# Kernel tuning notes

Hardware: AMD Instinct MI355X
Metric: run time of the kernel (lower is better)

Reference implementation:

```python
import jax, jax.numpy as jnp
import numpy as np

_SAMPLING_EPS = 1e-5
EOS_PROB_RATIO = 100.0
MIN_PROB_THRESHOLD = 0.001
MIX_RATIO = 0.5
EOS_TOKEN_ID = 2


def setup_inputs() -> dict:
    key = jax.random.key(0)
    k1, k2, k3, k4 = jax.random.split(key, 4)
    B, V = 256, 128000
    logits = jax.random.normal(k1, (B, V), dtype=jnp.float32) * 3.0
    # keep temperature away from 0 so the random-sampling path is exercised
    temperature = 0.2 + 1.3 * jax.random.uniform(k2, (B,), dtype=jnp.float32)
    top_p = 0.5 + 0.5 * jax.random.uniform(k3, (B,), dtype=jnp.float32)
    token_lengths = jax.random.randint(k4, (V,), 0, 20).astype(jnp.int32)
    return {
        "logits": logits,
        "temperature": temperature,
        "top_p": top_p,
        "token_lengths": token_lengths,
        "top_k": 50,
    }


def _apply_top_k_top_p(logits, top_k, top_p):
    """vLLM-style: ascending sort, top-k threshold, top-p cumulative mask, scatter back."""
    idx = jnp.argsort(logits, axis=-1)  # ascending
    lsort = jnp.take_along_axis(logits, idx, axis=-1)
    V = logits.shape[-1]
    # top-k: keep only the last top_k (largest) entries
    kth = lsort[:, V - top_k][:, None]
    lsort = jnp.where(lsort < kth, -jnp.inf, lsort)
    # top-p: mask low-cumulative-probability prefix (ascending order)
    probs = jax.nn.softmax(lsort, axis=-1)
    csum = jnp.cumsum(probs, axis=-1)
    pmask = csum <= (1.0 - top_p[:, None])
    pmask = pmask.at[:, -1].set(False)  # always keep the top token
    lsort = jnp.where(pmask, -jnp.inf, lsort)
    # scatter back to original token order
    inv = jnp.argsort(idx, axis=-1)
    return jnp.take_along_axis(lsort, inv, axis=-1)


def _longest_word_sample(logits, token_lengths, k, mix_ratio, eos_token_id):
    topk_logits, topk_idx = jax.lax.top_k(logits, k)  # [B,k]
    prob = jax.nn.softmax(topk_logits, axis=-1)
    lens = token_lengths[jnp.clip(topk_idx, 0, token_lengths.shape[0] - 1)].astype(jnp.float32)
    length_score = jax.nn.softmax(lens, axis=-1)
    mix = (1.0 - mix_ratio) * prob + mix_ratio * length_score
    mix = jnp.where(prob >= MIN_PROB_THRESHOLD, mix, -jnp.inf)
    # EOS threshold rule
    eos_in_topk = (topk_idx == eos_token_id) & jnp.isfinite(topk_logits)
    rows_with_eos = eos_in_topk.any(axis=-1, keepdims=True)
    eos_prob = jnp.sum(prob * eos_in_topk, axis=-1, keepdims=True)
    eos_thresh = jnp.maximum(eos_prob / EOS_PROB_RATIO, 0.005)
    valid = prob >= eos_thresh
    mix = jnp.where(valid | ~rows_with_eos, mix, -jnp.inf)
    best = jnp.argmax(mix, axis=-1)  # [B]
    chosen = jnp.take_along_axis(topk_idx, best[:, None], axis=-1)[:, 0]
    return chosen


def reference(logits, temperature, top_p, token_lengths, top_k):
    greedy = jnp.argmax(logits, axis=-1)
    scaled = logits / temperature[:, None]
    filtered = _apply_top_k_top_p(scaled, top_k, top_p)
    rnd = _longest_word_sample(filtered, token_lengths, top_k, MIX_RATIO, EOS_TOKEN_ID)
    sampled = jnp.where(temperature < _SAMPLING_EPS, greedy, rnd)
    return sampled.astype(jnp.int32)
```

## Files before the change

kernel.cpp:

```cpp
#include <hip/hip_runtime.h>
#include <stdint.h>
#include <math.h>

#define THREADS 1024
#define NBINS 8192
#define BIN_SHIFT 19
#define CAND_MAX 2048
#define MAXK 64
#define BATCH 16

__device__ __forceinline__ uint32_t fkey(float f) {
    uint32_t b = __float_as_uint(f);
    return (b & 0x80000000u) ? ~b : (b | 0x80000000u);
}
__device__ __forceinline__ float fval(uint32_t k) {
    uint32_t b = (k & 0x80000000u) ? (k & 0x7FFFFFFFu) : ~k;
    return __uint_as_float(b);
}

__global__ __launch_bounds__(THREADS, 1) void sampler_kernel(
    const float* __restrict__ logits,
    const float* __restrict__ temperature,
    const float* __restrict__ top_p,
    const int* __restrict__ token_lengths,
    const int* __restrict__ top_k_ptr,
    int* __restrict__ out, int V)
{
    const int row = blockIdx.x;
    const int tid = threadIdx.x;
    int K = *top_k_ptr;
    if (K < 1) K = 1;
    if (K > MAXK) K = MAXK;

    __shared__ uint32_t s_hist[NBINS];
    __shared__ uint32_t s_chunk[THREADS];
    __shared__ unsigned long long s_cand[CAND_MAX];
    __shared__ float s_vals[MAXK];
    __shared__ int s_idx[MAXK];
    __shared__ int s_slot[MAXK];
    __shared__ int s_T, s_cnt;

    for (int i = tid; i < NBINS; i += THREADS) s_hist[i] = 0u;
    if (tid == 0) s_cnt = 0;
    __syncthreads();

    const float* rowbase = logits + (size_t)row * (size_t)V;
    const int nv = V >> 2;
    const float4* rowp = reinterpret_cast<const float4*>(rowbase);
    const int jmax = nv - 1;

    for (int base = tid; base < nv; base += THREADS * BATCH) {
        float4 x[BATCH];
        #pragma unroll
        for (int b = 0; b < BATCH; ++b) {
            int j = base + b * THREADS;
            x[b] = rowp[(j < jmax) ? j : jmax];
        }
        #pragma unroll
        for (int b = 0; b < BATCH; ++b) {
            const int j = base + b * THREADS;
            if (j < nv) {
                atomicAdd(&s_hist[fkey(x[b].x) >> BIN_SHIFT], 1u);
                atomicAdd(&s_hist[fkey(x[b].y) >> BIN_SHIFT], 1u);
                atomicAdd(&s_hist[fkey(x[b].z) >> BIN_SHIFT], 1u);
                atomicAdd(&s_hist[fkey(x[b].w) >> BIN_SHIFT], 1u);
            }
        }
    }
    __syncthreads();

    const int CHUNK = NBINS / THREADS;
    {
        uint32_t cs = 0;
        const int base = tid * CHUNK;
        #pragma unroll
        for (int b = 0; b < CHUNK; ++b) cs += s_hist[base + b];
        s_chunk[tid] = cs;
    }
    __syncthreads();
    for (int off = 1; off < THREADS; off <<= 1) {
        uint32_t v = (tid + off < THREADS) ? s_chunk[tid + off] : 0u;
        __syncthreads();
        s_chunk[tid] += v;
        __syncthreads();
    }
    {
        uint32_t suf  = s_chunk[tid];
        uint32_t sufn = (tid + 1 < THREADS) ? s_chunk[tid + 1] : 0u;
        if (suf >= (uint32_t)K && sufn < (uint32_t)K) {
            uint32_t acc = sufn;
            int T = tid * CHUNK;
            for (int b = tid * CHUNK + CHUNK - 1; b >= tid * CHUNK; --b) {
                acc += s_hist[b];
                if (acc >= (uint32_t)K) { T = b; break; }
            }
            s_T = T;
        }
    }
    __syncthreads();

    const uint32_t T = (uint32_t)s_T;
    for (int base = tid; base < nv; base += THREADS * BATCH) {
        float4 x[BATCH];
        #pragma unroll
        for (int b = 0; b < BATCH; ++b) {
            int j = base + b * THREADS;
            x[b] = rowp[(j < jmax) ? j : jmax];
        }
        #pragma unroll
        for (int b = 0; b < BATCH; ++b) {
            const int j = base + b * THREADS;
            if (j < nv) {
                const uint32_t j4 = (uint32_t)(j << 2);
                uint32_t k;
                k = fkey(x[b].x); if ((k >> BIN_SHIFT) >= T) { int p = atomicAdd(&s_cnt, 1); if (p < CAND_MAX) s_cand[p] = ((unsigned long long)k << 32) | (uint32_t)~(j4 + 0u); }
                k = fkey(x[b].y); if ((k >> BIN_SHIFT) >= T) { int p = atomicAdd(&s_cnt, 1); if (p < CAND_MAX) s_cand[p] = ((unsigned long long)k << 32) | (uint32_t)~(j4 + 1u); }
                k = fkey(x[b].z); if ((k >> BIN_SHIFT) >= T) { int p = atomicAdd(&s_cnt, 1); if (p < CAND_MAX) s_cand[p] = ((unsigned long long)k << 32) | (uint32_t)~(j4 + 2u); }
                k = fkey(x[b].w); if ((k >> BIN_SHIFT) >= T) { int p = atomicAdd(&s_cnt, 1); if (p < CAND_MAX) s_cand[p] = ((unsigned long long)k << 32) | (uint32_t)~(j4 + 3u); }
            }
        }
    }
    __syncthreads();

    const int M = min(s_cnt, CAND_MAX);
    for (int t = tid; t < M; t += THREADS) {
        const unsigned long long mine = s_cand[t];
        int rank = 0;
        for (int j = 0; j < M; ++j) rank += (s_cand[j] > mine) ? 1 : 0;
        if (rank < MAXK) {
            s_idx[rank]  = (int)(~(uint32_t)mine);
            s_vals[rank] = fval((uint32_t)(mine >> 32));
        }
    }
    __syncthreads();

    if (tid >= 64) return;

    const float temp = temperature[row];
    const float tp   = top_p[row];

    const float a0 = s_vals[0] / temp;
    float e = 0.f;
    int myidx = -1;
    if (tid < K) {
        myidx = s_idx[tid];
        e = expf(s_vals[tid] / temp - a0);
    }
    float sum = e;
    #pragma unroll
    for (int off = 1; off < 64; off <<= 1) sum += __shfl_xor(sum, off, 64);
    const float p1 = e / sum;

    float cs = p1;
    #pragma unroll
    for (int off = 1; off < 64; off <<= 1) {
        float o = __shfl_down(cs, off, 64);
        cs += (tid + off < 64) ? o : 0.f;
    }
    const float lim = 1.0f - tp;
    const bool keep = (tid < K) && (tid == 0 || cs > lim);
    const int S = __popcll(__ballot(keep));

    float e2 = (tid < S) ? e : 0.f;
    float sum2 = e2;
    #pragma unroll
    for (int off = 1; off < 64; off <<= 1) sum2 += __shfl_xor(sum2, off, 64);
    const float p2 = e2 / sum2;

    const bool is_eos = (tid < S) && (myidx == 2);
    float eosp = is_eos ? p2 : 0.f;
    #pragma unroll
    for (int off = 1; off < 64; off <<= 1) eosp += __shfl_xor(eosp, off, 64);
    const bool has_eos = (__ballot(is_eos) != 0ull);
    const float eth = fmaxf(eosp / 100.0f, 0.005f);

    if (tid < S) s_slot[tid] = myidx;
    __builtin_amdgcn_wave_barrier();
    if (tid == 0) {
        unsigned long long m0 = 0ull, m1 = 0ull;
        for (int i = 0; i < S; ++i) {
            int id = s_idx[i];
            if (id < 64) m0 |= 1ull << id;
            else if (id < 128) m1 |= 1ull << (id - 64);
        }
        int nxt = 0;
        for (int i = S; i < K; ++i) {
            while ((nxt < 64) ? ((m0 >> nxt) & 1ull) : ((m1 >> (nxt - 64)) & 1ull)) nxt++;
            s_slot[i] = nxt++;
        }
    }
    __builtin_amdgcn_wave_barrier();

    float len = -INFINITY;
    if (tid < K) {
        int id = s_slot[tid];
        id = (id < 0) ? 0 : ((id >= V) ? V - 1 : id);
        len = (float)token_lengths[id];
    }
    float lmax = len;
    #pragma unroll
    for (int off = 1; off < 64; off <<= 1) lmax = fmaxf(lmax, __shfl_xor(lmax, off, 64));
    float el = (tid < K) ? expf(len - lmax) : 0.f;
    float lsum = el;
    #pragma unroll
    for (int off = 1; off < 64; off <<= 1) lsum += __shfl_xor(lsum, off, 64);
    const float ls = el / lsum;

    float mix = -INFINITY;
    if (tid < S) {
        mix = 0.5f * p2 + 0.5f * ls;
        if (!(p2 >= 0.001f)) mix = -INFINITY;
        if (has_eos && !(p2 >= eth)) mix = -INFINITY;
    }
    float bm = mix; int bi = tid;
    #pragma unroll
    for (int off = 1; off < 64; off <<= 1) {
        float om = __shfl_xor(bm, off, 64);
        int   oi = __shfl_xor(bi, off, 64);
        if (om > bm || (om == bm && oi < bi)) { bm = om; bi = oi; }
    }

    if (tid == 0) {
        int chosen = s_slot[bi];
        if (temp < 1e-5f) chosen = s_idx[0];
        out[row] = chosen;
    }
}

extern "C" void kernel_launch(void* const* d_in, const int* in_sizes, int n_in,
                              void* d_out, int out_size, void* d_ws, size_t ws_size,
                              hipStream_t stream) {
    const float* logits        = (const float*)d_in[0];
    const float* temperature   = (const float*)d_in[1];
    const float* top_p         = (const float*)d_in[2];
    const int*   token_lengths = (const int*)d_in[3];
    const int*   top_k_ptr     = (const int*)d_in[4];
    int* outp = (int*)d_out;

    const int B = in_sizes[1];
    const int V = in_sizes[3];

    sampler_kernel<<<B, THREADS, 0, stream>>>(logits, temperature, top_p,
                                              token_lengths, top_k_ptr, outp, V);
}
```

Before: 56.24 us.

## Stream logits through per-wave LDS ring via async global_load_lds and shuffle-based scan

Both passes over the row now use async global-to-LDS loads (global_load_lds) into a per-wave 4-slot ring buffer, with vmcnt waits, instead of batched float4 register loads. The goal is to overlap global memory latency with LDS atomics while cutting register pressure. The 1024-thread suffix scan, which needed many block-wide barriers, is replaced by wave-level shuffles plus one small cross-wave scan. CAND_MAX is reduced to make room for the staging buffer. The risk is that only three loads are in flight per wave, which may be less memory-level parallelism than the old 16-deep batches.

After: 51.55 us. -8.3%, faster.

```diff
diff --git a/kernel.cpp b/kernel.cpp
--- a/kernel.cpp
+++ b/kernel.cpp
@@ -3,11 +3,12 @@
 #include <math.h>
 
 #define THREADS 1024
+#define NWAVES 16
 #define NBINS 8192
 #define BIN_SHIFT 19
-#define CAND_MAX 2048
+#define CAND_MAX 1536
 #define MAXK 64
-#define BATCH 16
+#define RING 4
 
 __device__ __forceinline__ uint32_t fkey(float f) {
     uint32_t b = __float_as_uint(f);
@@ -16,6 +17,13 @@
 __device__ __forceinline__ float fval(uint32_t k) {
     uint32_t b = (k & 0x80000000u) ? (k & 0x7FFFFFFFu) : ~k;
     return __uint_as_float(b);
+}
+
+__device__ __forceinline__ void gload_lds16(const float* g, uint32_t* lds) {
+    __builtin_amdgcn_global_load_lds(
+        (const __attribute__((address_space(1))) void*)(const void*)g,
+        (__attribute__((address_space(3))) void*)(void*)lds,
+        16, 0, 0);
 }
 
 __global__ __launch_bounds__(THREADS, 1) void sampler_kernel(
@@ -26,18 +34,20 @@
     const int* __restrict__ top_k_ptr,
     int* __restrict__ out, int V)
 {
-    const int row = blockIdx.x;
-    const int tid = threadIdx.x;
+    const int row  = blockIdx.x;
+    const int tid  = threadIdx.x;
+    const int lane = tid & 63;
+    const int wid  = tid >> 6;
     int K = *top_k_ptr;
     if (K < 1) K = 1;
     if (K > MAXK) K = MAXK;
 
+    __shared__ __align__(16) uint32_t s_stage[NWAVES * RING * 256];
     __shared__ uint32_t s_hist[NBINS];
-    __shared__ uint32_t s_chunk[THREADS];
     __shared__ unsigned long long s_cand[CAND_MAX];
+    __shared__ uint32_t s_wsum[NWAVES], s_wtail[NWAVES];
     __shared__ float s_vals[MAXK];
-    __shared__ int s_idx[MAXK];
-    __shared__ int s_slot[MAXK];
+    __shared__ int s_idx[MAXK], s_slot[MAXK];
     __shared__ int s_T, s_cnt;
 
     for (int i = tid; i < NBINS; i += THREADS) s_hist[i] = 0u;
@@ -45,52 +55,74 @@
     __syncthreads();
 
     const float* rowbase = logits + (size_t)row * (size_t)V;
-    const int nv = V >> 2;
-    const float4* rowp = reinterpret_cast<const float4*>(rowbase);
-    const int jmax = nv - 1;
-
-    for (int base = tid; base < nv; base += THREADS * BATCH) {
-        float4 x[BATCH];
+    const int NREAL = (V + 255) >> 8;
+    const int NITER = (NREAL + NWAVES - 1) / NWAVES;
+    const int lastg = V - 4;
+    uint32_t* mystage = &s_stage[wid * (RING * 256)];
+
+    #pragma unroll
+    for (int k = 0; k < RING - 1; ++k) {
+        int ci = wid + NWAVES * k;
+        int c  = (ci < NREAL - 1) ? ci : (NREAL - 1);
+        int g  = c * 256 + lane * 4;
+        g = (g < lastg) ? g : lastg;
+        gload_lds16(rowbase + g, mystage + k * 256);
+    }
+    for (int i = 0; i < NITER; ++i) {
+        asm volatile("s_waitcnt vmcnt(2)" ::: "memory");
+        const uint32_t* sp = mystage + (i & (RING - 1)) * 256 + lane * 4;
+        float4 x = *reinterpret_cast<const float4*>(sp);
+        const int g0 = (wid + NWAVES * i) * 256 + lane * 4;
+        if (g0 < V) {
+            atomicAdd(&s_hist[fkey(x.x) >> BIN_SHIFT], 1u);
+            atomicAdd(&s_hist[fkey(x.y) >> BIN_SHIFT], 1u);
+            atomicAdd(&s_hist[fkey(x.z) >> BIN_SHIFT], 1u);
+            atomicAdd(&s_hist[fkey(x.w) >> BIN_SHIFT], 1u);
+        }
+        {
+            int ci = wid + NWAVES * (i + RING - 1);
+            int c  = (ci < NREAL - 1) ? ci : (NREAL - 1);
+            int g  = c * 256 + lane * 4;
+            g = (g < lastg) ? g : lastg;
+            gload_lds16(rowbase + g, mystage + ((i + RING - 1) & (RING - 1)) * 256);
+        }
+    }
+    asm volatile("s_waitcnt vmcnt(0)" ::: "memory");
+    __syncthreads();
+
+    const int CH = NBINS / THREADS;
+    uint32_t cs = 0;
+    {
+        const int b0 = tid * CH;
         #pragma unroll
-        for (int b = 0; b < BATCH; ++b) {
-            int j = base + b * THREADS;
-            x[b] = rowp[(j < jmax) ? j : jmax];
-        }
+        for (int b = 0; b < CH; ++b) cs += s_hist[b0 + b];
+    }
+    uint32_t suf = cs;
+    #pragma unroll
+    for (int off = 1; off < 64; off <<= 1) {
+        uint32_t o = __shfl_down(suf, off, 64);
+        suf += (lane + off < 64) ? o : 0u;
+    }
+    if (lane == 0) s_wsum[wid] = suf;
+    __syncthreads();
+    if (wid == 0 && lane < NWAVES) {
+        uint32_t t = s_wsum[lane];
+        uint32_t s = t;
         #pragma unroll
-        for (int b = 0; b < BATCH; ++b) {
-            const int j = base + b * THREADS;
-            if (j < nv) {
-                atomicAdd(&s_hist[fkey(x[b].x) >> BIN_SHIFT], 1u);
-                atomicAdd(&s_hist[fkey(x[b].y) >> BIN_SHIFT], 1u);
-                atomicAdd(&s_hist[fkey(x[b].z) >> BIN_SHIFT], 1u);
-                atomicAdd(&s_hist[fkey(x[b].w) >> BIN_SHIFT], 1u);
-            }
-        }
-    }
-    __syncthreads();
-
-    const int CHUNK = NBINS / THREADS;
+        for (int off = 1; off < NWAVES; off <<= 1) {
+            uint32_t o = __shfl_down(s, off, 64);
+            s += (lane + off < NWAVES) ? o : 0u;
+        }
+        s_wtail[lane] = s - t;
+    }
+    __syncthreads();
     {
-        uint32_t cs = 0;
-        const int base = tid * CHUNK;
-        #pragma unroll
-        for (int b = 0; b < CHUNK; ++b) cs += s_hist[base + b];
-        s_chunk[tid] = cs;
-    }
-    __syncthreads();
-    for (int off = 1; off < THREADS; off <<= 1) {
-        uint32_t v = (tid + off < THREADS) ? s_chunk[tid + off] : 0u;
-        __syncthreads();
-        s_chunk[tid] += v;
-        __syncthreads();
-    }
-    {
-        uint32_t suf  = s_chunk[tid];
-        uint32_t sufn = (tid + 1 < THREADS) ? s_chunk[tid + 1] : 0u;
-        if (suf >= (uint32_t)K && sufn < (uint32_t)K) {
+        uint32_t sufg = suf + s_wtail[wid];
+        uint32_t sufn = sufg - cs;
+        if (sufg >= (uint32_t)K && sufn < (uint32_t)K) {
             uint32_t acc = sufn;
-            int T = tid * CHUNK;
-            for (int b = tid * CHUNK + CHUNK - 1; b >= tid * CHUNK; --b) {
+            int T = tid * CH;
+            for (int b = tid * CH + CH - 1; b >= tid * CH; --b) {
                 acc += s_hist[b];
                 if (acc >= (uint32_t)K) { T = b; break; }
             }
@@ -100,29 +132,38 @@
     __syncthreads();
 
     const uint32_t T = (uint32_t)s_T;
-    for (int base = tid; base < nv; base += THREADS * BATCH) {
-        float4 x[BATCH];
-        #pragma unroll
-        for (int b = 0; b < BATCH; ++b) {
-            int j = base + b * THREADS;
-            x[b] = rowp[(j < jmax) ? j : jmax];
-        }
-        #pragma unroll
-        for (int b = 0; b < BATCH; ++b) {
-            const int j = base + b * THREADS;
-            if (j < nv) {
-                const uint32_t j4 = (uint32_t)(j << 2);
-                uint32_t k;
-                k = fkey(x[b].x); if ((k >> BIN_SHIFT) >= T) { int p = atomicAdd(&s_cnt, 1); if (p < CAND_MAX) s_cand[p] = ((unsigned long long)k << 32) | (uint32_t)~(j4 + 0u); }
-                k = fkey(x[b].y); if ((k >> BIN_SHIFT) >= T) { int p = atomicAdd(&s_cnt, 1); if (p < CAND_MAX) s_cand[p] = ((unsigned long long)k << 32) | (uint32_t)~(j4 + 1u); }
-                k = fkey(x[b].z); if ((k >> BIN_SHIFT) >= T) { int p = atomicAdd(&s_cnt, 1); if (p < CAND_MAX) s_cand[p] = ((unsigned long long)k << 32) | (uint32_t)~(j4 + 2u); }
-                k = fkey(x[b].w); if ((k >> BIN_SHIFT) >= T) { int p = atomicAdd(&s_cnt, 1); if (p < CAND_MAX) s_cand[p] = ((unsigned long long)k << 32) | (uint32_t)~(j4 + 3u); }
-            }
-        }
-    }
-    __syncthreads();
-
-    const int M = min(s_cnt, CAND_MAX);
+    #pragma unroll
+    for (int k = 0; k < RING - 1; ++k) {
+        int ci = wid + NWAVES * k;
+        int c  = (ci < NREAL - 1) ? ci : (NREAL - 1);
+        int g  = c * 256 + lane * 4;
+        g = (g < lastg) ? g : lastg;
+        gload_lds16(rowbase + g, mystage + k * 256);
+    }
+    for (int i = 0; i < NITER; ++i) {
+        asm volatile("s_waitcnt vmcnt(2)" ::: "memory");
+        const uint32_t* sp = mystage + (i & (RING - 1)) * 256 + lane * 4;
+        float4 x = *reinterpret_cast<const float4*>(sp);
+        const int g0 = (wid + NWAVES * i) * 256 + lane * 4;
+        if (g0 < V) {
+            uint32_t k0;
+            k0 = fkey(x.x); if ((k0 >> BIN_SHIFT) >= T) { int p = atomicAdd(&s_cnt, 1); if (p < CAND_MAX) s_cand[p] = ((unsigned long long)k0 << 32) | (uint32_t)~(uint32_t)(g0 + 0); }
+            k0 = fkey(x.y); if ((k0 >> BIN_SHIFT) >= T) { int p = atomicAdd(&s_cnt, 1); if (p < CAND_MAX) s_cand[p] = ((unsigned long long)k0 << 32) | (uint32_t)~(uint32_t)(g0 + 1); }
+            k0 = fkey(x.z); if ((k0 >> BIN_SHIFT) >= T) { int p = atomicAdd(&s_cnt, 1); if (p < CAND_MAX) s_cand[p] = ((unsigned long long)k0 << 32) | (uint32_t)~(uint32_t)(g0 + 2); }
+            k0 = fkey(x.w); if ((k0 >> BIN_SHIFT) >= T) { int p = atomicAdd(&s_cnt, 1); if (p < CAND_MAX) s_cand[p] = ((unsigned long long)k0 << 32) | (uint32_t)~(uint32_t)(g0 + 3); }
+        }
+        {
+            int ci = wid + NWAVES * (i + RING - 1);
+            int c  = (ci < NREAL - 1) ? ci : (NREAL - 1);
+            int g  = c * 256 + lane * 4;
+            g = (g < lastg) ? g : lastg;
+            gload_lds16(rowbase + g, mystage + ((i + RING - 1) & (RING - 1)) * 256);
+        }
+    }
+    asm volatile("s_waitcnt vmcnt(0)" ::: "memory");
+    __syncthreads();
+
+    const int M = (s_cnt < CAND_MAX) ? s_cnt : CAND_MAX;
     for (int t = tid; t < M; t += THREADS) {
         const unsigned long long mine = s_cand[t];
         int rank = 0;
@@ -151,14 +192,14 @@
     for (int off = 1; off < 64; off <<= 1) sum += __shfl_xor(sum, off, 64);
     const float p1 = e / sum;
 
-    float cs = p1;
+    float csf = p1;
     #pragma unroll
     for (int off = 1; off < 64; off <<= 1) {
-        float o = __shfl_down(cs, off, 64);
-        cs += (tid + off < 64) ? o : 0.f;
+        float o = __shfl_down(csf, off, 64);
+        csf += (tid + off < 64) ? o : 0.f;
     }
     const float lim = 1.0f - tp;
-    const bool keep = (tid < K) && (tid == 0 || cs > lim);
+    const bool keep = (tid < K) && (tid == 0 || csf > lim);
     const int S = __popcll(__ballot(keep));
 
     float e2 = (tid < S) ? e : 0.f;
```
